# Kernel optimization log

Hardware: AMD Instinct MI355X
Metric: run time of the kernel (lower is better)

Reference implementation:

```python
import jax, jax.numpy as jnp
import numpy as np

N_NODES = 50000
N_EDGES = 640000
HIDDEN = 128
N_LAYERS = 4
NUM_RBF = 50
CUTOFF = 4.0
N_GRAPHS = 64
VOCAB = 128
LN_EPS = 1e-5


def setup_inputs() -> dict:
    key = jax.random.key(0)
    ks = jax.random.split(key, 16)
    s = 1.0 / np.sqrt(HIDDEN)
    sr = 1.0 / np.sqrt(NUM_RBF)
    inp = {
        "x": jax.random.randint(ks[0], (N_NODES,), 0, VOCAB, dtype=jnp.int64) if jax.config.jax_enable_x64 else jax.random.randint(ks[0], (N_NODES,), 0, VOCAB).astype(jnp.int32),
        "edge_index": jax.random.randint(ks[1], (2, N_EDGES), 0, N_NODES).astype(jnp.int32),
        "edge_attr": jax.random.uniform(ks[2], (N_EDGES,), dtype=jnp.float32) * CUTOFF,
        "batch": jnp.sort(jax.random.randint(ks[3], (N_NODES,), 0, N_GRAPHS)).astype(jnp.int32),
        # embedding table
        "emb": jax.random.normal(ks[4], (VOCAB, HIDDEN), dtype=jnp.float32),
        # filter net: Linear(num_rbf, H) -> ReLU -> Linear(H, H), stacked over layers
        "fw1": jax.random.normal(ks[5], (N_LAYERS, NUM_RBF, HIDDEN), dtype=jnp.float32) * sr,
        "fb1": jnp.zeros((N_LAYERS, HIDDEN), dtype=jnp.float32),
        "fw2": jax.random.normal(ks[6], (N_LAYERS, HIDDEN, HIDDEN), dtype=jnp.float32) * s,
        "fb2": jnp.zeros((N_LAYERS, HIDDEN), dtype=jnp.float32),
        # lin: Linear(H, H) per layer
        "lw": jax.random.normal(ks[7], (N_LAYERS, HIDDEN, HIDDEN), dtype=jnp.float32) * s,
        "lb": jnp.zeros((N_LAYERS, HIDDEN), dtype=jnp.float32),
        # LayerNorm params per layer
        "ln_g": jnp.ones((N_LAYERS, HIDDEN), dtype=jnp.float32),
        "ln_b": jnp.zeros((N_LAYERS, HIDDEN), dtype=jnp.float32),
    }
    return inp


def _gaussian_smearing(dist):
    offset = jnp.linspace(0.0, CUTOFF, NUM_RBF, dtype=jnp.float32)  # [R]
    coeff = -0.5 / (CUTOFF / (NUM_RBF - 1)) ** 2
    d = dist[:, None] - offset[None, :]  # [E, R]
    return jnp.exp(coeff * d * d)


def _layer_norm(h, g, b):
    mu = jnp.mean(h, axis=-1, keepdims=True)
    var = jnp.mean(jnp.square(h - mu), axis=-1, keepdims=True)
    return (h - mu) * jax.lax.rsqrt(var + LN_EPS) * g + b


def reference(x, edge_index, edge_attr, batch, emb, fw1, fb1, fw2, fb2, lw, lb, ln_g, ln_b):
    edge_rbf = _gaussian_smearing(edge_attr)          # [E, R]
    h = emb[x]                                        # [N, H]
    row, col = edge_index[0], edge_index[1]
    for i in range(N_LAYERS):
        # FilterNet(RBF): [E, H]
        w = jax.nn.relu(edge_rbf @ fw1[i] + fb1[i]) @ fw2[i] + fb2[i]
        xl = h @ lw[i] + lb[i]                        # [N, H]
        msg = xl[col] * w                             # gather + elementwise, [E, H]
        out = jax.ops.segment_sum(msg, row, num_segments=N_NODES)
        h = _layer_norm(h + out, ln_g[i], ln_b[i])
    # global mean pool over graphs
    sums = jax.ops.segment_sum(h, batch, num_segments=N_GRAPHS)      # [G, H]
    cnt = jax.ops.segment_sum(jnp.ones((N_NODES,), h.dtype), batch, num_segments=N_GRAPHS)
    return sums / jnp.maximum(cnt, 1.0)[:, None]
```

## Files before the change

### kernel.cpp

```cpp
#include <hip/hip_runtime.h>
#include <hip/hip_bf16.h>

#define N_NODES 50000
#define N_EDGES 640000
#define HIDDEN 128
#define N_LAYERS 4
#define NUM_RBF 50
#define CUTOFF 4.0f
#define N_GRAPHS 64
#define TAB 8192
#define TG 8
#define PSPLIT 16
#define COLBITS 17
#define NBUCK 196
#define CHUNK 4096

typedef unsigned int uint;
typedef unsigned short ushort;
typedef __attribute__((ext_vector_type(8))) short bf16x8;
typedef __attribute__((ext_vector_type(4))) float f32x4;

__device__ inline ushort f2bf(float f) {
    uint u = __float_as_uint(f);
    uint r = (u + 0x7fffu + ((u >> 16) & 1u)) >> 16;
    return (ushort)r;
}
__device__ inline uint packbf(float lo, float hi) {
    return (uint)f2bf(lo) | ((uint)f2bf(hi) << 16);
}
__device__ inline float bflo(uint u) { return __uint_as_float(u << 16); }
__device__ inline float bfhi(uint u) { return __uint_as_float(u & 0xffff0000u); }

__global__ __launch_bounds__(128) void k_table(const float* __restrict__ fw1,
                                               const float* __restrict__ fb1,
                                               const float* __restrict__ fw2,
                                               const float* __restrict__ fb2,
                                               uint* __restrict__ ctab) {
    int bid = blockIdx.x;
    int layer = bid / (TAB / TG);
    int g0 = (bid % (TAB / TG)) * TG;
    int j = threadIdx.x;
    __shared__ float rbf[TG][NUM_RBF];
    __shared__ float wout[TG][HIDDEN];
    __shared__ float hid[TG][HIDDEN];
    for (int idx = j; idx < TG * NUM_RBF; idx += 128) {
        int gg = idx / NUM_RBF, r = idx % NUM_RBF;
        float d = (CUTOFF * (g0 + gg)) / (float)(TAB - 1);
        float offset = (CUTOFF * r) / (float)(NUM_RBF - 1);
        float delta = CUTOFF / (float)(NUM_RBF - 1);
        float coeff = -0.5f / (delta * delta);
        float t = d - offset;
        rbf[gg][r] = expf(coeff * t * t);
    }
    __syncthreads();
    const float* w1 = fw1 + layer * NUM_RBF * HIDDEN;
    float b1 = fb1[layer * HIDDEN + j];
    float acc[TG];
    #pragma unroll
    for (int gg = 0; gg < TG; gg++) acc[gg] = b1;
    for (int r = 0; r < NUM_RBF; r++) {
        float w = w1[r * HIDDEN + j];
        #pragma unroll
        for (int gg = 0; gg < TG; gg++) acc[gg] = fmaf(rbf[gg][r], w, acc[gg]);
    }
    #pragma unroll
    for (int gg = 0; gg < TG; gg++) hid[gg][j] = fmaxf(acc[gg], 0.0f);
    __syncthreads();
    const float* w2 = fw2 + layer * HIDDEN * HIDDEN;
    float b2 = fb2[layer * HIDDEN + j];
    float acc2[TG];
    #pragma unroll
    for (int gg = 0; gg < TG; gg++) acc2[gg] = b2;
    for (int k = 0; k < HIDDEN; k += 4) {
        float w0 = w2[(k + 0) * HIDDEN + j];
        float w1v = w2[(k + 1) * HIDDEN + j];
        float w2v = w2[(k + 2) * HIDDEN + j];
        float w3 = w2[(k + 3) * HIDDEN + j];
        #pragma unroll
        for (int gg = 0; gg < TG; gg++) {
            acc2[gg] = fmaf(hid[gg][k + 0], w0, acc2[gg]);
            acc2[gg] = fmaf(hid[gg][k + 1], w1v, acc2[gg]);
            acc2[gg] = fmaf(hid[gg][k + 2], w2v, acc2[gg]);
            acc2[gg] = fmaf(hid[gg][k + 3], w3, acc2[gg]);
        }
    }
    #pragma unroll
    for (int gg = 0; gg < TG; gg++) wout[gg][j] = acc2[gg];
    __syncthreads();
    for (int idx = j; idx < TG * 64; idx += 128) {
        int gg = idx >> 6, jp = idx & 63;
        ctab[((size_t)layer * TAB + g0 + gg) * 64 + jp] =
            packbf(wout[gg][2 * jp], wout[gg][2 * jp + 1]);
    }
}

__global__ void k_embed(const int* __restrict__ x, const float* __restrict__ emb,
                        ushort* __restrict__ hbf) {
    int idx = blockIdx.x * 256 + threadIdx.x;
    if (idx >= N_NODES * 32) return;
    int n = idx >> 5, q = idx & 31;
    float4 v = ((const float4*)emb)[x[n] * 32 + q];
    uint2 p;
    p.x = packbf(v.x, v.y);
    p.y = packbf(v.z, v.w);
    ((uint2*)hbf)[idx] = p;
}

__global__ void k_packw(const float* __restrict__ lw, uint4* __restrict__ pb) {
    int idx = blockIdx.x * 256 + threadIdx.x;
    if (idx >= N_LAYERS * 8 * 4 * 64) return;
    int lane = idx & 63;
    int kc = (idx >> 6) & 3;
    int nt = (idx >> 8) & 7;
    int layer = idx >> 11;
    int quad = lane >> 4, nl = lane & 15;
    int n = nt * 16 + nl;
    const float* w = lw + layer * HIDDEN * HIDDEN;
    uint r[4];
    #pragma unroll
    for (int jj = 0; jj < 4; jj++) {
        int k = kc * 32 + quad * 8 + 2 * jj;
        r[jj] = packbf(w[k * HIDDEN + n], w[(k + 1) * HIDDEN + n]);
    }
    uint4 o; o.x = r[0]; o.y = r[1]; o.z = r[2]; o.w = r[3];
    pb[idx] = o;
}

__global__ void k_count(const int* __restrict__ row, int* __restrict__ counts) {
    int e = blockIdx.x * 256 + threadIdx.x;
    if (e < N_EDGES) atomicAdd(&counts[row[e]], 1);
}

__global__ void k_scan1(const int* __restrict__ counts, int* __restrict__ partial,
                        int* __restrict__ blocksum) {
    int i = blockIdx.x * 256 + threadIdx.x;
    int v = (i < N_NODES) ? counts[i] : 0;
    int lane = threadIdx.x & 63;
    int wid = threadIdx.x >> 6;
    int s = v;
    #pragma unroll
    for (int off = 1; off < 64; off <<= 1) {
        int t = __shfl_up(s, off, 64);
        if (lane >= off) s += t;
    }
    __shared__ int wsum[4];
    if (lane == 63) wsum[wid] = s;
    __syncthreads();
    int woff = 0;
    for (int w = 0; w < wid; w++) woff += wsum[w];
    int incl = s + woff;
    if (i < N_NODES) partial[i] = incl - v;
    if (threadIdx.x == 255) blocksum[blockIdx.x] = incl;
}

__global__ void k_scan2(int* __restrict__ blocksum, int nblk) {
    int tid = threadIdx.x;
    int v = (tid < nblk) ? blocksum[tid] : 0;
    int lane = tid & 63, wid = tid >> 6;
    int s = v;
    #pragma unroll
    for (int off = 1; off < 64; off <<= 1) {
        int t = __shfl_up(s, off, 64);
        if (lane >= off) s += t;
    }
    __shared__ int wsum[4];
    if (lane == 63) wsum[wid] = s;
    __syncthreads();
    int woff = 0;
    for (int w = 0; w < wid; w++) woff += wsum[w];
    int incl = s + woff;
    if (tid < nblk) blocksum[tid] = incl - v;
}

__global__ void k_scan3(const int* __restrict__ partial, const int* __restrict__ blocksum,
                        int* __restrict__ offsets, int* __restrict__ bcur) {
    int i = blockIdx.x * 256 + threadIdx.x;
    if (i < N_NODES) {
        int o = partial[i] + blocksum[blockIdx.x];
        offsets[i] = o;
        if ((i & 255) == 0) bcur[i >> 8] = o;
    }
    if (i == 0) offsets[N_NODES] = N_EDGES;
}

__global__ __launch_bounds__(256) void k_bucket(const int* __restrict__ row,
                                                const int* __restrict__ col,
                                                const float* __restrict__ eattr,
                                                int* __restrict__ bcur,
                                                uint2* __restrict__ bs) {
    __shared__ uint2 stage[CHUNK];
    __shared__ int hist[256], lscan[256], lcur[256], gbase[256];
    __shared__ int wsum[4];
    int t = threadIdx.x;
    int e0 = blockIdx.x * CHUNK;
    int ne = min(CHUNK, N_EDGES - e0);
    hist[t] = 0;
    __syncthreads();
    for (int i = t; i < ne; i += 256)
        atomicAdd(&hist[row[e0 + i] >> 8], 1);
    __syncthreads();
    int v = hist[t];
    int lane = t & 63, wid = t >> 6;
    int s = v;
    #pragma unroll
    for (int off = 1; off < 64; off <<= 1) {
        int u = __shfl_up(s, off, 64);
        if (lane >= off) s += u;
    }
    if (lane == 63) wsum[wid] = s;
    __syncthreads();
    int woff = 0;
    for (int w = 0; w < wid; w++) woff += wsum[w];
    int excl = s + woff - v;
    lscan[t] = excl;
    lcur[t] = excl;
    if (v > 0) gbase[t] = atomicAdd(&bcur[t], v);
    __syncthreads();
    for (int i = t; i < ne; i += 256) {
        int e = e0 + i;
        int r = row[e];
        float tt = eattr[e] * ((float)(TAB - 1) / CUTOFF);
        int gi = (int)(tt + 0.5f);
        gi = min(max(gi, 0), TAB - 1);
        int pos = atomicAdd(&lcur[r >> 8], 1);
        uint2 sv;
        sv.x = (uint)col[e] | ((uint)gi << COLBITS);
        sv.y = (uint)r;
        stage[pos] = sv;
    }
    __syncthreads();
    for (int i = t; i < ne; i += 256) {
        uint2 sv = stage[i];
        int b = sv.y >> 8;
        bs[gbase[b] + (i - lscan[b])] = sv;
    }
}

__global__ __launch_bounds__(256) void k_scatter(const uint2* __restrict__ bs,
                                                 const int* __restrict__ offsets,
                                                 uint* __restrict__ meta) {
    int b = blockIdx.x, t = threadIdx.x;
    int r0 = b << 8;
    __shared__ int cur[256];
    int rmax = min(r0 + 256, N_NODES);
    cur[t] = offsets[min(r0 + t, N_NODES)];
    __syncthreads();
    int s = offsets[r0], e = offsets[rmax];
    for (int i = s + t; i < e; i += 256) {
        uint2 v = bs[i];
        int slot = atomicAdd(&cur[v.y - r0], 1);
        meta[slot] = v.x;
    }
}

__global__ __launch_bounds__(256) void k_xl(const ushort* __restrict__ hbf,
                                            const uint4* __restrict__ pb,
                                            const float* __restrict__ lb,
                                            ushort* __restrict__ xlb) {
    int wave = threadIdx.x >> 6, lane = threadIdx.x & 63;
    int m0 = (blockIdx.x * 4 + wave) * 16;
    if (m0 >= N_NODES) return;
    int quad = lane >> 4, ml = lane & 15;
    const ushort* arow = hbf + (size_t)(m0 + ml) * HIDDEN + quad * 8;
    bf16x8 a[4];
    #pragma unroll
    for (int kc = 0; kc < 4; kc++) a[kc] = *(const bf16x8*)(arow + kc * 32);
    #pragma unroll
    for (int nt = 0; nt < 8; nt++) {
        f32x4 acc = {0.f, 0.f, 0.f, 0.f};
        #pragma unroll
        for (int kc = 0; kc < 4; kc++) {
            bf16x8 b = *(const bf16x8*)(pb + (nt * 4 + kc) * 64 + lane);
            acc = __builtin_amdgcn_mfma_f32_16x16x32_bf16(a[kc], b, acc, 0, 0, 0);
        }
        int col = nt * 16 + ml;
        float bias = lb[col];
        #pragma unroll
        for (int r = 0; r < 4; r++) {
            int row = m0 + quad * 4 + r;
            xlb[(size_t)row * HIDDEN + col] = f2bf(acc[r] + bias);
        }
    }
}

__global__ __launch_bounds__(256) void k_agg(const ushort* __restrict__ xlb,
                                             const uint* __restrict__ meta,
                                             const int* __restrict__ offsets,
                                             const uint* __restrict__ ctab,
                                             const ushort* __restrict__ hb_in,
                                             const float* __restrict__ g,
                                             const float* __restrict__ b,
                                             ushort* __restrict__ hbf_out) {
    int wid = threadIdx.x >> 6;
    int lane = threadIdx.x & 63;
    int n = blockIdx.x * 4 + wid;
    if (n >= N_NODES) return;
    const uint* xl2 = (const uint*)xlb;
    float accx = 0.f, accy = 0.f;
    int p0 = offsets[n], p1 = offsets[n + 1];
    int cnt = p1 - p0;
    for (int base = 0; base < cnt; base += 64) {
        int li = p0 + base + lane;
        uint mlv = meta[min(li, N_EDGES - 1)];
        int kk = min(64, cnt - base);
        int k4 = kk & ~3;
        int p = 0;
        for (; p < k4; p += 4) {
            uint m0 = __builtin_amdgcn_readlane(mlv, p + 0);
            uint m1 = __builtin_amdgcn_readlane(mlv, p + 1);
            uint m2 = __builtin_amdgcn_readlane(mlv, p + 2);
            uint m3 = __builtin_amdgcn_readlane(mlv, p + 3);
            uint w0 = ctab[(m0 >> COLBITS) * 64 + lane];
            uint w1 = ctab[(m1 >> COLBITS) * 64 + lane];
            uint w2 = ctab[(m2 >> COLBITS) * 64 + lane];
            uint w3 = ctab[(m3 >> COLBITS) * 64 + lane];
            uint x0 = xl2[(m0 & ((1u << COLBITS) - 1)) * 64 + lane];
            uint x1 = xl2[(m1 & ((1u << COLBITS) - 1)) * 64 + lane];
            uint x2 = xl2[(m2 & ((1u << COLBITS) - 1)) * 64 + lane];
            uint x3 = xl2[(m3 & ((1u << COLBITS) - 1)) * 64 + lane];
            accx = fmaf(bflo(w0), bflo(x0), accx);
            accy = fmaf(bfhi(w0), bfhi(x0), accy);
            accx = fmaf(bflo(w1), bflo(x1), accx);
            accy = fmaf(bfhi(w1), bfhi(x1), accy);
            accx = fmaf(bflo(w2), bflo(x2), accx);
            accy = fmaf(bfhi(w2), bfhi(x2), accy);
            accx = fmaf(bflo(w3), bflo(x3), accx);
            accy = fmaf(bfhi(w3), bfhi(x3), accy);
        }
        for (; p < kk; p++) {
            uint m = __builtin_amdgcn_readlane(mlv, p);
            uint w = ctab[(m >> COLBITS) * 64 + lane];
            uint xv = xl2[(m & ((1u << COLBITS) - 1)) * 64 + lane];
            accx = fmaf(bflo(w), bflo(xv), accx);
            accy = fmaf(bfhi(w), bfhi(xv), accy);
        }
    }
    uint hvp = ((const uint*)hb_in)[n * 64 + lane];
    float vx = bflo(hvp) + accx, vy = bfhi(hvp) + accy;
    float s = vx + vy;
    #pragma unroll
    for (int off = 32; off; off >>= 1) s += __shfl_xor(s, off, 64);
    float mu = s * (1.0f / 128.0f);
    float dx = vx - mu, dy = vy - mu;
    float s2 = dx * dx + dy * dy;
    #pragma unroll
    for (int off = 32; off; off >>= 1) s2 += __shfl_xor(s2, off, 64);
    float rstd = rsqrtf(s2 * (1.0f / 128.0f) + 1e-5f);
    float2 gv = ((const float2*)g)[lane];
    float2 bv = ((const float2*)b)[lane];
    float ox = fmaf(dx * rstd, gv.x, bv.x);
    float oy = fmaf(dy * rstd, gv.y, bv.y);
    ((uint*)hbf_out)[n * 64 + lane] = packbf(ox, oy);
}

__global__ void k_bounds(const int* __restrict__ batch, int* __restrict__ gstart) {
    int g = threadIdx.x;
    if (g > N_GRAPHS) return;
    int lo = 0, hi = N_NODES;
    while (lo < hi) {
        int mid = (lo + hi) >> 1;
        if (batch[mid] < g) lo = mid + 1; else hi = mid;
    }
    gstart[g] = lo;
}

__global__ __launch_bounds__(256) void k_pool_part(const ushort* __restrict__ hbf,
                                                   const int* __restrict__ gstart,
                                                   float* __restrict__ partial) {
    int g = blockIdx.x / PSPLIT;
    int t = blockIdx.x % PSPLIT;
    int jp = threadIdx.x & 63;
    int half = threadIdx.x >> 6;
    int s = gstart[g], e = gstart[g + 1];
    float accx = 0.f, accy = 0.f;
    const uint* h2 = (const uint*)hbf;
    for (int n = s + t * 4 + half; n < e; n += PSPLIT * 4) {
        uint v = h2[n * 64 + jp];
        accx += bflo(v);
        accy += bfhi(v);
    }
    __shared__ float redx[256], redy[256];
    redx[threadIdx.x] = accx;
    redy[threadIdx.x] = accy;
    __syncthreads();
    if (half == 0) {
        float tx = redx[jp] + redx[jp + 64] + redx[jp + 128] + redx[jp + 192];
        float ty = redy[jp] + redy[jp + 64] + redy[jp + 128] + redy[jp + 192];
        float2 o; o.x = tx; o.y = ty;
        ((float2*)partial)[(g * PSPLIT + t) * 64 + jp] = o;
    }
}

__global__ void k_pool_fin(const float* __restrict__ partial,
                           const int* __restrict__ gstart,
                           float* __restrict__ out) {
    int idx = blockIdx.x * 128 + threadIdx.x;
    int g = idx >> 7, j = idx & 127;
    float tot = 0.f;
    #pragma unroll
    for (int t = 0; t < PSPLIT; t++) tot += partial[(g * PSPLIT + t) * HIDDEN + j];
    float c = (float)(gstart[g + 1] - gstart[g]);
    out[idx] = tot / fmaxf(c, 1.0f);
}

extern "C" void kernel_launch(void* const* d_in, const int* in_sizes, int n_in,
                              void* d_out, int out_size, void* d_ws, size_t ws_size,
                              hipStream_t stream) {
    const int* x = (const int*)d_in[0];
    const int* edge_index = (const int*)d_in[1];
    const int* row = edge_index;
    const int* col = edge_index + N_EDGES;
    const float* eattr = (const float*)d_in[2];
    const int* batch = (const int*)d_in[3];
    const float* emb = (const float*)d_in[4];
    const float* fw1 = (const float*)d_in[5];
    const float* fb1 = (const float*)d_in[6];
    const float* fw2 = (const float*)d_in[7];
    const float* fb2 = (const float*)d_in[8];
    const float* lw = (const float*)d_in[9];
    const float* lb = (const float*)d_in[10];
    const float* ln_g = (const float*)d_in[11];
    const float* ln_b = (const float*)d_in[12];
    float* out = (float*)d_out;

    char* ws = (char*)d_ws;
    size_t off = 0;
    auto alloc = [&](size_t bytes) -> void* {
        void* p = ws + off;
        off = (off + bytes + 255) & ~(size_t)255;
        return p;
    };
    uint* ctab     = (uint*)alloc((size_t)N_LAYERS * TAB * 64 * 4);
    ushort* hbf_a  = (ushort*)alloc((size_t)N_NODES * HIDDEN * 2);
    ushort* hbf_b  = (ushort*)alloc((size_t)N_NODES * HIDDEN * 2);
    ushort* xlb    = (ushort*)alloc((size_t)N_NODES * HIDDEN * 2);
    uint4* pb      = (uint4*)alloc((size_t)N_LAYERS * 8 * 4 * 64 * 16);
    int* counts    = (int*)alloc((size_t)(N_NODES + 1) * 4);
    int* offsets   = (int*)alloc((size_t)(N_NODES + 1) * 4);
    int* partial   = (int*)alloc((size_t)N_NODES * 4);
    int* blocksum  = (int*)alloc(256 * 4);
    int* bcur      = (int*)alloc(256 * 4);
    uint2* bs      = (uint2*)alloc((size_t)N_EDGES * 8);
    uint* meta     = (uint*)alloc((size_t)N_EDGES * 4);
    int* gstart    = (int*)alloc((size_t)(N_GRAPHS + 1) * 4);
    float* ppart   = (float*)alloc((size_t)N_GRAPHS * PSPLIT * HIDDEN * 4);

    hipMemsetAsync(counts, 0, (size_t)(N_NODES + 1) * 4, stream);

    k_table<<<N_LAYERS * (TAB / TG), 128, 0, stream>>>(fw1, fb1, fw2, fb2, ctab);
    k_embed<<<(N_NODES * 32 + 255) / 256, 256, 0, stream>>>(x, emb, hbf_a);
    k_packw<<<(N_LAYERS * 8 * 4 * 64 + 255) / 256, 256, 0, stream>>>(lw, pb);
    k_count<<<(N_EDGES + 255) / 256, 256, 0, stream>>>(row, counts);
    const int NBLK = (N_NODES + 255) / 256;
    k_scan1<<<NBLK, 256, 0, stream>>>(counts, partial, blocksum);
    k_scan2<<<1, 256, 0, stream>>>(blocksum, NBLK);
    k_scan3<<<NBLK, 256, 0, stream>>>(partial, blocksum, offsets, bcur);
    k_bucket<<<(N_EDGES + CHUNK - 1) / CHUNK, 256, 0, stream>>>(row, col, eattr, bcur, bs);
    k_scatter<<<NBUCK, 256, 0, stream>>>(bs, offsets, meta);
    k_bounds<<<1, 128, 0, stream>>>(batch, gstart);

    ushort* hb_cur = hbf_a; ushort* hb_nxt = hbf_b;
    const int XLBLK = (N_NODES / 16 + 3) / 4;
    for (int i = 0; i < N_LAYERS; i++) {
        k_xl<<<XLBLK, 256, 0, stream>>>(hb_cur, pb + (size_t)i * 8 * 4 * 64,
                                        lb + i * HIDDEN, xlb);
        k_agg<<<(N_NODES + 3) / 4, 256, 0, stream>>>(xlb, meta, offsets,
                                                     ctab + (size_t)i * TAB * 64,
                                                     hb_cur, ln_g + i * HIDDEN,
                                                     ln_b + i * HIDDEN, hb_nxt);
        ushort* tb = hb_cur; hb_cur = hb_nxt; hb_nxt = tb;
    }
    k_pool_part<<<N_GRAPHS * PSPLIT, 256, 0, stream>>>(hb_cur, gstart, ppart);
    k_pool_fin<<<(N_GRAPHS * HIDDEN + 127) / 128, 128, 0, stream>>>(ppart, gstart, out);
}
```

Before: 401.7 us.

## Split filter table build and compute second layer with bf16 MFMA

The filter-net lookup table build is split into two kernels. The first computes the RBF hidden layer and stores it as bf16. The second runs the 128x128 second linear layer with MFMA 16x16x32 bf16 instructions, using fw2 packed by the existing packing kernel. This replaces a scalar FP32 FMA loop with matrix cores. In exchange it adds an intermediate buffer round trip and two extra launches, and it rounds the hidden activations to bf16 before the second matmul.

Result: faster. 384.3 us (-4.3%).

```diff
diff --git a/kernel.cpp b/kernel.cpp
--- a/kernel.cpp
+++ b/kernel.cpp
@@ -31,18 +31,14 @@
 __device__ inline float bflo(uint u) { return __uint_as_float(u << 16); }
 __device__ inline float bfhi(uint u) { return __uint_as_float(u & 0xffff0000u); }
 
-__global__ __launch_bounds__(128) void k_table(const float* __restrict__ fw1,
-                                               const float* __restrict__ fb1,
-                                               const float* __restrict__ fw2,
-                                               const float* __restrict__ fb2,
-                                               uint* __restrict__ ctab) {
+__global__ __launch_bounds__(128) void k_tab1(const float* __restrict__ fw1,
+                                              const float* __restrict__ fb1,
+                                              ushort* __restrict__ hidbf) {
     int bid = blockIdx.x;
     int layer = bid / (TAB / TG);
     int g0 = (bid % (TAB / TG)) * TG;
     int j = threadIdx.x;
     __shared__ float rbf[TG][NUM_RBF];
-    __shared__ float wout[TG][HIDDEN];
-    __shared__ float hid[TG][HIDDEN];
     for (int idx = j; idx < TG * NUM_RBF; idx += 128) {
         int gg = idx / NUM_RBF, r = idx % NUM_RBF;
         float d = (CUTOFF * (g0 + gg)) / (float)(TAB - 1);
@@ -64,33 +60,39 @@
         for (int gg = 0; gg < TG; gg++) acc[gg] = fmaf(rbf[gg][r], w, acc[gg]);
     }
     #pragma unroll
-    for (int gg = 0; gg < TG; gg++) hid[gg][j] = fmaxf(acc[gg], 0.0f);
-    __syncthreads();
-    const float* w2 = fw2 + layer * HIDDEN * HIDDEN;
-    float b2 = fb2[layer * HIDDEN + j];
-    float acc2[TG];
-    #pragma unroll
-    for (int gg = 0; gg < TG; gg++) acc2[gg] = b2;
-    for (int k = 0; k < HIDDEN; k += 4) {
-        float w0 = w2[(k + 0) * HIDDEN + j];
-        float w1v = w2[(k + 1) * HIDDEN + j];
-        float w2v = w2[(k + 2) * HIDDEN + j];
-        float w3 = w2[(k + 3) * HIDDEN + j];
+    for (int gg = 0; gg < TG; gg++)
+        hidbf[((size_t)layer * TAB + g0 + gg) * HIDDEN + j] = f2bf(fmaxf(acc[gg], 0.0f));
+}
+
+__global__ __launch_bounds__(256) void k_tab2(const ushort* __restrict__ hidbf,
+                                              const uint4* __restrict__ pb2,
+                                              const float* __restrict__ fb2,
+                                              ushort* __restrict__ ctab) {
+    int wave = threadIdx.x >> 6, lane = threadIdx.x & 63;
+    int m0 = (blockIdx.x * 4 + wave) * 16;
+    int layer = m0 / TAB;
+    int quad = lane >> 4, ml = lane & 15;
+    const ushort* arow = hidbf + (size_t)(m0 + ml) * HIDDEN + quad * 8;
+    bf16x8 a[4];
+    #pragma unroll
+    for (int kc = 0; kc < 4; kc++) a[kc] = *(const bf16x8*)(arow + kc * 32);
+    const uint4* pb = pb2 + (size_t)layer * 8 * 4 * 64;
+    const float* bias = fb2 + layer * HIDDEN;
+    #pragma unroll
+    for (int nt = 0; nt < 8; nt++) {
+        f32x4 acc = {0.f, 0.f, 0.f, 0.f};
         #pragma unroll
-        for (int gg = 0; gg < TG; gg++) {
-            acc2[gg] = fmaf(hid[gg][k + 0], w0, acc2[gg]);
-            acc2[gg] = fmaf(hid[gg][k + 1], w1v, acc2[gg]);
-            acc2[gg] = fmaf(hid[gg][k + 2], w2v, acc2[gg]);
-            acc2[gg] = fmaf(hid[gg][k + 3], w3, acc2[gg]);
-        }
-    }
-    #pragma unroll
-    for (int gg = 0; gg < TG; gg++) wout[gg][j] = acc2[gg];
-    __syncthreads();
-    for (int idx = j; idx < TG * 64; idx += 128) {
-        int gg = idx >> 6, jp = idx & 63;
-        ctab[((size_t)layer * TAB + g0 + gg) * 64 + jp] =
-            packbf(wout[gg][2 * jp], wout[gg][2 * jp + 1]);
+        for (int kc = 0; kc < 4; kc++) {
+            bf16x8 b = *(const bf16x8*)(pb + (nt * 4 + kc) * 64 + lane);
+            acc = __builtin_amdgcn_mfma_f32_16x16x32_bf16(a[kc], b, acc, 0, 0, 0);
+        }
+        int col = nt * 16 + ml;
+        float bv = bias[col];
+        #pragma unroll
+        for (int r = 0; r < 4; r++) {
+            int row = m0 + quad * 4 + r;
+            ctab[(size_t)row * HIDDEN + col] = f2bf(acc[r] + bv);
+        }
     }
 }
 
@@ -106,7 +108,7 @@
     ((uint2*)hbf)[idx] = p;
 }
 
-__global__ void k_packw(const float* __restrict__ lw, uint4* __restrict__ pb) {
+__global__ void k_packw(const float* __restrict__ w_in, uint4* __restrict__ pb) {
     int idx = blockIdx.x * 256 + threadIdx.x;
     if (idx >= N_LAYERS * 8 * 4 * 64) return;
     int lane = idx & 63;
@@ -115,7 +117,7 @@
     int layer = idx >> 11;
     int quad = lane >> 4, nl = lane & 15;
     int n = nt * 16 + nl;
-    const float* w = lw + layer * HIDDEN * HIDDEN;
+    const float* w = w_in + layer * HIDDEN * HIDDEN;
     uint r[4];
     #pragma unroll
     for (int jj = 0; jj < 4; jj++) {
@@ -431,10 +433,12 @@
         return p;
     };
     uint* ctab     = (uint*)alloc((size_t)N_LAYERS * TAB * 64 * 4);
+    ushort* hidbf  = (ushort*)alloc((size_t)N_LAYERS * TAB * HIDDEN * 2);
     ushort* hbf_a  = (ushort*)alloc((size_t)N_NODES * HIDDEN * 2);
     ushort* hbf_b  = (ushort*)alloc((size_t)N_NODES * HIDDEN * 2);
     ushort* xlb    = (ushort*)alloc((size_t)N_NODES * HIDDEN * 2);
     uint4* pb      = (uint4*)alloc((size_t)N_LAYERS * 8 * 4 * 64 * 16);
+    uint4* pb2     = (uint4*)alloc((size_t)N_LAYERS * 8 * 4 * 64 * 16);
     int* counts    = (int*)alloc((size_t)(N_NODES + 1) * 4);
     int* offsets   = (int*)alloc((size_t)(N_NODES + 1) * 4);
     int* partial   = (int*)alloc((size_t)N_NODES * 4);
@@ -447,9 +451,11 @@
 
     hipMemsetAsync(counts, 0, (size_t)(N_NODES + 1) * 4, stream);
 
-    k_table<<<N_LAYERS * (TAB / TG), 128, 0, stream>>>(fw1, fb1, fw2, fb2, ctab);
+    k_packw<<<(N_LAYERS * 8 * 4 * 64 + 255) / 256, 256, 0, stream>>>(lw, pb);
+    k_packw<<<(N_LAYERS * 8 * 4 * 64 + 255) / 256, 256, 0, stream>>>(fw2, pb2);
+    k_tab1<<<N_LAYERS * (TAB / TG), 128, 0, stream>>>(fw1, fb1, hidbf);
+    k_tab2<<<(N_LAYERS * TAB) / 64, 256, 0, stream>>>(hidbf, pb2, fb2, (ushort*)ctab);
     k_embed<<<(N_NODES * 32 + 255) / 256, 256, 0, stream>>>(x, emb, hbf_a);
-    k_packw<<<(N_LAYERS * 8 * 4 * 64 + 255) / 256, 256, 0, stream>>>(lw, pb);
     k_count<<<(N_EDGES + 255) / 256, 256, 0, stream>>>(row, counts);
     const int NBLK = (N_NODES + 255) / 256;
     k_scan1<<<NBLK, 256, 0, stream>>>(counts, partial, blocksum);
```
